# Performance work log

Hardware: AMD Instinct MI355X
Metric: run time of the kernel (lower is better)

## Reference

```python
import jax, jax.numpy as jnp
import numpy as np

N = 50000   # nodes
E = 800000  # edges


def gcn_conv(x, src, dst, W, b):
    # PyG GCNConv: h = x @ W; add self-loops; symmetric norm D^-1/2 A D^-1/2; + bias
    h = x @ W                                              # [N, dout]
    deg = jax.ops.segment_sum(jnp.ones((E,), h.dtype), dst, num_segments=N) + 1.0  # +1 self-loop
    inv_sqrt = jax.lax.rsqrt(deg)                          # [N]
    coef = inv_sqrt[src] * inv_sqrt[dst]                   # [E]
    agg = jax.ops.segment_sum(h[src] * coef[:, None], dst, num_segments=N)
    agg = agg + h * (inv_sqrt * inv_sqrt)[:, None]         # self-loop contribution
    return agg + b


def setup_inputs() -> dict:
    key = jax.random.key(0)
    ks = jax.random.split(key, 6)
    x = jax.random.normal(ks[0], (N, 128), jnp.float32)
    edge_index = jax.random.randint(ks[1], (2, E), 0, N, jnp.int32)
    W1 = jax.random.normal(ks[2], (128, 128), jnp.float32) * (1.0 / np.sqrt(128.0))
    b1 = jnp.zeros((128,), jnp.float32)
    W2 = jax.random.normal(ks[3], (128, 64), jnp.float32) * (1.0 / np.sqrt(128.0))
    b2 = jnp.zeros((64,), jnp.float32)
    return {"x": x, "edge_index": edge_index, "W1": W1, "b1": b1, "W2": W2, "b2": b2}


def reference(x, edge_index, W1, b1, W2, b2):
    src, dst = edge_index[0], edge_index[1]
    h = jax.nn.relu(gcn_conv(x, src, dst, W1, b1))
    # dropout is identity in eval mode (training=False)
    return gcn_conv(h, src, dst, W2, b2)
```

## Files before the change

kernel.cpp:

```cpp
#include <hip/hip_runtime.h>

typedef unsigned int uint32;
typedef unsigned short ushort16;

__device__ __forceinline__ ushort16 f2bf(float f) {
    union { float f; uint32 u; } v; v.f = f;
    uint32 r = v.u + 0x7fffu + ((v.u >> 16) & 1u);
    return (ushort16)(r >> 16);
}
__device__ __forceinline__ float bflo(uint32 u) {
    union { uint32 u; float f; } v; v.u = u << 16; return v.f;
}
__device__ __forceinline__ float bfhi(uint32 u) {
    union { uint32 u; float f; } v; v.u = u & 0xffff0000u; return v.f;
}

#define BSH 6
#define NBMAX 1024
#define CHUNK 4096


__global__ void k_zerob(int* __restrict__ b, int nb) {
    int i = blockIdx.x * 256 + threadIdx.x;
    if (i < nb) b[i] = 0;
}

__global__ __launch_bounds__(256) void k_bcount(const int* __restrict__ dst,
                                                int* __restrict__ bcnt, int e, int nb) {
    __shared__ int cnt[NBMAX];
    for (int i = threadIdx.x; i < nb; i += 256) cnt[i] = 0;
    __syncthreads();
    int base = blockIdx.x * CHUNK;
    int end = min(e, base + CHUNK);
    for (int i = base + threadIdx.x; i < end; i += 256)
        atomicAdd(&cnt[dst[i] >> BSH], 1);
    __syncthreads();
    for (int i = threadIdx.x; i < nb; i += 256) {
        int c = cnt[i];
        if (c) atomicAdd(&bcnt[i], c);
    }
}

__global__ void k_bscan(const int* __restrict__ bcnt, int* __restrict__ bstart,
                        int* __restrict__ bcur, int nb, int e) {
    __shared__ int s[256];
    __shared__ int carry;
    int tid = threadIdx.x;
    if (tid == 0) carry = 0;
    __syncthreads();
    for (int base = 0; base < nb; base += 256) {
        int v = (base + tid < nb) ? bcnt[base + tid] : 0;
        s[tid] = v;
        __syncthreads();
        for (int off = 1; off < 256; off <<= 1) {
            int t = (tid >= off) ? s[tid - off] : 0;
            __syncthreads();
            s[tid] += t;
            __syncthreads();
        }
        int ex = s[tid] - v + carry;
        if (base + tid < nb) { bstart[base + tid] = ex; bcur[base + tid] = ex; }
        __syncthreads();
        if (tid == 0) carry += s[255];
        __syncthreads();
    }
    if (tid == 0) bstart[nb] = e;
}

__global__ __launch_bounds__(256) void k_binA2(const int* __restrict__ src,
                                               const int* __restrict__ dst,
                                               int* __restrict__ bcur,
                                               int2* __restrict__ rec, int e, int nb) {
    __shared__ int cnt[NBMAX];
    __shared__ int bas[NBMAX];
    __shared__ int off[NBMAX];
    for (int i = threadIdx.x; i < nb; i += 256) { cnt[i] = 0; off[i] = 0; }
    __syncthreads();
    int base = blockIdx.x * CHUNK;
    int end = min(e, base + CHUNK);
    for (int i = base + threadIdx.x; i < end; i += 256)
        atomicAdd(&cnt[dst[i] >> BSH], 1);
    __syncthreads();
    for (int i = threadIdx.x; i < nb; i += 256) {
        int c = cnt[i];
        if (c) bas[i] = atomicAdd(&bcur[i], c);
    }
    __syncthreads();
    for (int i = base + threadIdx.x; i < end; i += 256) {
        int s = src[i];
        int d = dst[i];
        int b = d >> BSH;
        int p = bas[b] + atomicAdd(&off[b], 1);
        rec[p] = make_int2(s, d);
    }
}

__global__ __launch_bounds__(256) void k_degB(const int2* __restrict__ rec,
                                              const int* __restrict__ bstart,
                                              int* __restrict__ rowstart,
                                              float* __restrict__ inv, int n, int e) {
    __shared__ int cnt[64];
    int b = blockIdx.x;
    int st = bstart[b], en = bstart[b + 1];
    if (threadIdx.x < 64) cnt[threadIdx.x] = 0;
    __syncthreads();
    for (int i = st + threadIdx.x; i < en; i += 256)
        atomicAdd(&cnt[rec[i].y & 63], 1);
    __syncthreads();
    if (threadIdx.x < 64) {
        int c = cnt[threadIdx.x];
        int incl = c;
        #pragma unroll
        for (int o2 = 1; o2 < 64; o2 <<= 1) {
            int t = __shfl_up(incl, o2, 64);
            if ((int)threadIdx.x >= o2) incl += t;
        }
        int node = (b << BSH) + threadIdx.x;
        if (node < n) {
            rowstart[node] = st + incl - c;
            inv[node] = rsqrtf((float)c + 1.0f);
        }
    }
    if (b == 0 && threadIdx.x == 0) rowstart[n] = e;
}

__global__ __launch_bounds__(256) void k_fillB2(const int2* __restrict__ rec,
                                                const int* __restrict__ bstart,
                                                const int* __restrict__ rowstart,
                                                const float* __restrict__ inv,
                                                int2* __restrict__ es, int n) {
    __shared__ int cur[64];
    int b = blockIdx.x;
    int st = bstart[b], en = bstart[b + 1];
    if (threadIdx.x < 64) {
        int node = (b << BSH) + threadIdx.x;
        cur[threadIdx.x] = (node < n) ? (rowstart[node] - st) : 0;
    }
    __syncthreads();
    for (int i = st + threadIdx.x; i < en; i += 256) {
        int2 r = rec[i];
        int slot = atomicAdd(&cur[r.y & 63], 1);
        es[st + slot] = make_int2(r.x, __float_as_int(inv[r.x]));
    }
}


__global__ __launch_bounds__(256) void k_gemm1(const float* __restrict__ x,
                                               const float* __restrict__ W,
                                               ushort16* __restrict__ h, int n) {
    __shared__ float sW[128 * 128];
    __shared__ float sx[32 * 128];
    int tid = threadIdx.x;
    for (int i = tid * 4; i < 128 * 128; i += 1024)
        *(float4*)&sW[i] = *(const float4*)&W[i];
    int row0 = blockIdx.x * 32;
    for (int i = tid * 4; i < 32 * 128; i += 1024) {
        int r = row0 + (i >> 7);
        float4 v = (r < n) ? *(const float4*)&x[r * 128 + (i & 127)]
                           : make_float4(0.f, 0.f, 0.f, 0.f);
        *(float4*)&sx[i] = v;
    }
    __syncthreads();
    int c4 = (tid & 31) * 4;
    int rg = tid >> 5;
    float4 acc[4] = {};
    #pragma unroll 4
    for (int k = 0; k < 128; ++k) {
        float4 wv = *(const float4*)&sW[k * 128 + c4];
        #pragma unroll
        for (int i = 0; i < 4; ++i) {
            float xv = sx[(rg + 8 * i) * 128 + k];
            acc[i].x += xv * wv.x; acc[i].y += xv * wv.y;
            acc[i].z += xv * wv.z; acc[i].w += xv * wv.w;
        }
    }
    #pragma unroll
    for (int i = 0; i < 4; ++i) {
        int r = row0 + rg + 8 * i;
        if (r < n) {
            uint32 lo = (uint32)f2bf(acc[i].x) | ((uint32)f2bf(acc[i].y) << 16);
            uint32 hi = (uint32)f2bf(acc[i].z) | ((uint32)f2bf(acc[i].w) << 16);
            *(uint2*)&h[r * 128 + c4] = make_uint2(lo, hi);
        }
    }
}

__global__ __launch_bounds__(256) void k_gemm2(const float* __restrict__ a,
                                               const float* __restrict__ W,
                                               ushort16* __restrict__ h, int n) {
    __shared__ float sW[128 * 64];
    __shared__ float sx[64 * 128];
    int tid = threadIdx.x;
    for (int i = tid * 4; i < 128 * 64; i += 1024)
        *(float4*)&sW[i] = *(const float4*)&W[i];
    int row0 = blockIdx.x * 64;
    for (int i = tid * 4; i < 64 * 128; i += 1024) {
        int r = row0 + (i >> 7);
        float4 v = (r < n) ? *(const float4*)&a[r * 128 + (i & 127)]
                           : make_float4(0.f, 0.f, 0.f, 0.f);
        *(float4*)&sx[i] = v;
    }
    __syncthreads();
    int c4 = (tid & 15) * 4;
    int rg = tid >> 4;
    float4 acc[4] = {};
    #pragma unroll 4
    for (int k = 0; k < 128; ++k) {
        float4 wv = *(const float4*)&sW[k * 64 + c4];
        #pragma unroll
        for (int i = 0; i < 4; ++i) {
            float xv = sx[(rg + 16 * i) * 128 + k];
            acc[i].x += xv * wv.x; acc[i].y += xv * wv.y;
            acc[i].z += xv * wv.z; acc[i].w += xv * wv.w;
        }
    }
    #pragma unroll
    for (int i = 0; i < 4; ++i) {
        int r = row0 + rg + 16 * i;
        if (r < n) {
            uint32 lo = (uint32)f2bf(acc[i].x) | ((uint32)f2bf(acc[i].y) << 16);
            uint32 hi = (uint32)f2bf(acc[i].z) | ((uint32)f2bf(acc[i].w) << 16);
            *(uint2*)&h[r * 64 + c4] = make_uint2(lo, hi);
        }
    }
}

template <int COLS, bool RELU>
__global__ __launch_bounds__(256) void k_gather(const ushort16* __restrict__ h,
                                                const int* __restrict__ rowstart,
                                                const int2* __restrict__ es,
                                                const float* __restrict__ inv,
                                                const float* __restrict__ bias,
                                                float* __restrict__ out, int n) {
    int wave = threadIdx.x >> 6;
    int lane = threadIdx.x & 63;
    int node = blockIdx.x * 4 + wave;
    if (node >= n) return;
    int s0 = rowstart[node];
    int s1 = rowstart[node + 1];
    float iv = inv[node];

    if constexpr (COLS == 128) {
        int c = lane * 2;
        float accx = 0.f, accy = 0.f;
        int i = s0;
        for (; i + 8 <= s1; i += 8) {
            int   a[8];
            float w[8];
            uint32 u[8];
            #pragma unroll
            for (int j = 0; j < 8; ++j) {
                int2 r = es[i + j];
                a[j] = r.x;
                w[j] = __int_as_float(r.y);
            }
            #pragma unroll
            for (int j = 0; j < 8; ++j)
                u[j] = *(const uint32*)&h[(size_t)a[j] * 128 + c];
            #pragma unroll
            for (int j = 0; j < 8; ++j) {
                accx += w[j] * bflo(u[j]);
                accy += w[j] * bfhi(u[j]);
            }
        }
        for (; i < s1; ++i) {
            int2 r = es[i];
            uint32 u = *(const uint32*)&h[(size_t)r.x * 128 + c];
            float w = __int_as_float(r.y);
            accx += w * bflo(u);
            accy += w * bfhi(u);
        }
        uint32 us = *(const uint32*)&h[(size_t)node * 128 + c];
        float2 bb = *(const float2*)&bias[c];
        float ox = iv * accx + iv * iv * bflo(us) + bb.x;
        float oy = iv * accy + iv * iv * bfhi(us) + bb.y;
        if (RELU) { ox = fmaxf(ox, 0.f); oy = fmaxf(oy, 0.f); }
        *(float2*)&out[node * 128 + c] = make_float2(ox, oy);
    } else {
        int c = lane;
        float acc = 0.f;
        int i = s0;
        for (; i + 8 <= s1; i += 8) {
            int   a[8];
            float w[8];
            ushort16 u[8];
            #pragma unroll
            for (int j = 0; j < 8; ++j) {
                int2 r = es[i + j];
                a[j] = r.x;
                w[j] = __int_as_float(r.y);
            }
            #pragma unroll
            for (int j = 0; j < 8; ++j)
                u[j] = h[(size_t)a[j] * 64 + c];
            #pragma unroll
            for (int j = 0; j < 8; ++j)
                acc += w[j] * bflo((uint32)u[j]);
        }
        for (; i < s1; ++i) {
            int2 r = es[i];
            acc += __int_as_float(r.y) * bflo((uint32)h[(size_t)r.x * 64 + c]);
        }
        float self = bflo((uint32)h[(size_t)node * 64 + c]);
        float o = iv * acc + iv * iv * self + bias[c];
        if (RELU) o = fmaxf(o, 0.f);
        out[node * 64 + c] = o;
    }
}


extern "C" void kernel_launch(void* const* d_in, const int* in_sizes, int n_in,
                              void* d_out, int out_size, void* d_ws, size_t ws_size,
                              hipStream_t stream) {
    const float* x  = (const float*)d_in[0];
    const int*   ei = (const int*)d_in[1];
    const float* W1 = (const float*)d_in[2];
    const float* b1 = (const float*)d_in[3];
    const float* W2 = (const float*)d_in[4];
    const float* b2 = (const float*)d_in[5];
    float* out = (float*)d_out;

    const int N = in_sizes[0] / 128;
    const int E = in_sizes[1] / 2;
    const int NB = (N + 63) >> BSH;
    const int* src = ei;
    const int* dstp = ei + E;

    char* p = (char*)d_ws;
    auto take = [&](size_t bytes) {
        char* r = p;
        p += (bytes + 255) & ~(size_t)255;
        return r;
    };
    float*    inv      = (float*)take((size_t)N * 4);
    int*      rowstart = (int*)take((size_t)(N + 1) * 4);
    int*      bcnt     = (int*)take((size_t)NB * 4);
    int*      bstart   = (int*)take((size_t)(NB + 1) * 4);
    int*      bcur     = (int*)take((size_t)NB * 4);
    int2*     rec      = (int2*)take((size_t)E * 8);
    int2*     es       = (int2*)take((size_t)E * 8);
    ushort16* h1       = (ushort16*)take((size_t)N * 128 * 2);
    float*    act1     = (float*)take((size_t)N * 128 * 4);
    ushort16* h2       = (ushort16*)h1;

    const int nbC = (E + CHUNK - 1) / CHUNK;

    k_zerob <<<(NB + 255) / 256, 256, 0, stream>>>(bcnt, NB);
    k_bcount<<<nbC, 256, 0, stream>>>(dstp, bcnt, E, NB);
    k_bscan <<<1, 256, 0, stream>>>(bcnt, bstart, bcur, NB, E);
    k_binA2 <<<nbC, 256, 0, stream>>>(src, dstp, bcur, rec, E, NB);
    k_degB  <<<NB, 256, 0, stream>>>(rec, bstart, rowstart, inv, N, E);
    k_fillB2<<<NB, 256, 0, stream>>>(rec, bstart, rowstart, inv, es, N);

    k_gemm1<<<(N + 31) / 32, 256, 0, stream>>>(x, W1, h1, N);
    k_gather<128, true><<<(N + 3) / 4, 256, 0, stream>>>(h1, rowstart, es, inv, b1, act1, N);
    k_gemm2<<<(N + 63) / 64, 256, 0, stream>>>(act1, W2, h2, N);
    k_gather<64, false><<<(N + 3) / 4, 256, 0, stream>>>(h2, rowstart, es, inv, b2, out, N);
}
```

Baseline: 259.5 us.

## Replace scalar FP32 GEMMs with split-bf16 MFMA GEMMs

```diff
diff --git a/kernel.cpp b/kernel.cpp
--- a/kernel.cpp
+++ b/kernel.cpp
@@ -1,17 +1,19 @@
 #include <hip/hip_runtime.h>
 
 typedef unsigned int uint32;
-typedef unsigned short ushort16;
-
-__device__ __forceinline__ ushort16 f2bf(float f) {
+typedef unsigned short ush;
+typedef __attribute__((ext_vector_type(8))) short short8;
+typedef __attribute__((ext_vector_type(4))) float f32x4;
+
+__device__ __forceinline__ ush f2bf(float f) {
     union { float f; uint32 u; } v; v.f = f;
     uint32 r = v.u + 0x7fffu + ((v.u >> 16) & 1u);
-    return (ushort16)(r >> 16);
-}
-__device__ __forceinline__ float bflo(uint32 u) {
+    return (ush)(r >> 16);
+}
+__device__ __forceinline__ float bfl(uint32 u) {
     union { uint32 u; float f; } v; v.u = u << 16; return v.f;
 }
-__device__ __forceinline__ float bfhi(uint32 u) {
+__device__ __forceinline__ float bfh(uint32 u) {
     union { uint32 u; float f; } v; v.u = u & 0xffff0000u; return v.f;
 }
 
@@ -144,89 +146,120 @@
     }
 }
 
-
-__global__ __launch_bounds__(256) void k_gemm1(const float* __restrict__ x,
-                                               const float* __restrict__ W,
-                                               ushort16* __restrict__ h, int n) {
-    __shared__ float sW[128 * 128];
-    __shared__ float sx[32 * 128];
+__global__ void k_wcvt(const float* __restrict__ W, ush* __restrict__ wh,
+                       ush* __restrict__ wl, int csh, int total) {
+    int i = blockIdx.x * 256 + threadIdx.x;
+    if (i >= total) return;
+    int k = i >> csh;
+    int col = i & ((1 << csh) - 1);
+    float w = W[i];
+    ush hi = f2bf(w);
+    ush lo = f2bf(w - bfl((uint32)hi));
+    int byte = ((col * 128 + k) * 2) ^ ((col & 7) << 4);
+    *(ush*)((char*)wh + byte) = hi;
+    *(ush*)((char*)wl + byte) = lo;
+}
+
+template <int COUT>
+__global__ __launch_bounds__(256) void k_gemm_mfma(const float* __restrict__ x,
+                                                   const ush* __restrict__ gwh,
+                                                   const ush* __restrict__ gwl,
+                                                   ush* __restrict__ h, int n) {
+    constexpr int CT = COUT / 32;
+    __shared__ short xh[128 * 128];
+    __shared__ short xl[128 * 128];
+    __shared__ short wh[COUT * 128];
+    __shared__ short wl[COUT * 128];
     int tid = threadIdx.x;
-    for (int i = tid * 4; i < 128 * 128; i += 1024)
-        *(float4*)&sW[i] = *(const float4*)&W[i];
-    int row0 = blockIdx.x * 32;
-    for (int i = tid * 4; i < 32 * 128; i += 1024) {
-        int r = row0 + (i >> 7);
-        float4 v = (r < n) ? *(const float4*)&x[r * 128 + (i & 127)]
-                           : make_float4(0.f, 0.f, 0.f, 0.f);
-        *(float4*)&sx[i] = v;
-    }
-    __syncthreads();
-    int c4 = (tid & 31) * 4;
-    int rg = tid >> 5;
-    float4 acc[4] = {};
-    #pragma unroll 4
-    for (int k = 0; k < 128; ++k) {
-        float4 wv = *(const float4*)&sW[k * 128 + c4];
-        #pragma unroll
-        for (int i = 0; i < 4; ++i) {
-            float xv = sx[(rg + 8 * i) * 128 + k];
-            acc[i].x += xv * wv.x; acc[i].y += xv * wv.y;
-            acc[i].z += xv * wv.z; acc[i].w += xv * wv.w;
-        }
+    int row0 = blockIdx.x * 128;
+
+    for (int i = tid; i < COUT * 16; i += 256) {
+        ((short8*)wh)[i] = ((const short8*)gwh)[i];
+        ((short8*)wl)[i] = ((const short8*)gwl)[i];
     }
     #pragma unroll
-    for (int i = 0; i < 4; ++i) {
-        int r = row0 + rg + 8 * i;
-        if (r < n) {
-            uint32 lo = (uint32)f2bf(acc[i].x) | ((uint32)f2bf(acc[i].y) << 16);
-            uint32 hi = (uint32)f2bf(acc[i].z) | ((uint32)f2bf(acc[i].w) << 16);
-            *(uint2*)&h[r * 128 + c4] = make_uint2(lo, hi);
-        }
-    }
-}
-
-__global__ __launch_bounds__(256) void k_gemm2(const float* __restrict__ a,
-                                               const float* __restrict__ W,
-                                               ushort16* __restrict__ h, int n) {
-    __shared__ float sW[128 * 64];
-    __shared__ float sx[64 * 128];
-    int tid = threadIdx.x;
-    for (int i = tid * 4; i < 128 * 64; i += 1024)
-        *(float4*)&sW[i] = *(const float4*)&W[i];
-    int row0 = blockIdx.x * 64;
-    for (int i = tid * 4; i < 64 * 128; i += 1024) {
-        int r = row0 + (i >> 7);
-        float4 v = (r < n) ? *(const float4*)&a[r * 128 + (i & 127)]
-                           : make_float4(0.f, 0.f, 0.f, 0.f);
-        *(float4*)&sx[i] = v;
-    }
-    __syncthreads();
-    int c4 = (tid & 15) * 4;
-    int rg = tid >> 4;
-    float4 acc[4] = {};
-    #pragma unroll 4
-    for (int k = 0; k < 128; ++k) {
-        float4 wv = *(const float4*)&sW[k * 64 + c4];
-        #pragma unroll
-        for (int i = 0; i < 4; ++i) {
-            float xv = sx[(rg + 16 * i) * 128 + k];
-            acc[i].x += xv * wv.x; acc[i].y += xv * wv.y;
-            acc[i].z += xv * wv.z; acc[i].w += xv * wv.w;
-        }
-    }
+    for (int i = 0; i < 8; ++i) {
+        int rl = (tid >> 4) + i * 16;
+        int k0 = (tid & 15) * 8;
+        int row = row0 + rl;
+        float f[8];
+        if (row < n) {
+            float4 p0 = *(const float4*)&x[(size_t)row * 128 + k0];
+            float4 p1 = *(const float4*)&x[(size_t)row * 128 + k0 + 4];
+            f[0] = p0.x; f[1] = p0.y; f[2] = p0.z; f[3] = p0.w;
+            f[4] = p1.x; f[5] = p1.y; f[6] = p1.z; f[7] = p1.w;
+        } else {
+            #pragma unroll
+            for (int j = 0; j < 8; ++j) f[j] = 0.f;
+        }
+        short8 hi, lo;
+        #pragma unroll
+        for (int j = 0; j < 8; ++j) {
+            ush hb = f2bf(f[j]);
+            hi[j] = (short)hb;
+            lo[j] = (short)f2bf(f[j] - bfl((uint32)hb));
+        }
+        int byte = (rl * 256 + k0 * 2) ^ ((rl & 7) << 4);
+        *(short8*)((char*)xh + byte) = hi;
+        *(short8*)((char*)xl + byte) = lo;
+    }
+    __syncthreads();
+
+    int wid = tid >> 6, lane = tid & 63;
+    int wr = wid >> 1, wc = wid & 1;
+    int arow = wr * 64;
+    int bcol = wc * (COUT / 2);
+    int l15 = lane & 15, kg = lane >> 4;
+
+    f32x4 acc[4][CT];
     #pragma unroll
-    for (int i = 0; i < 4; ++i) {
-        int r = row0 + rg + 16 * i;
-        if (r < n) {
-            uint32 lo = (uint32)f2bf(acc[i].x) | ((uint32)f2bf(acc[i].y) << 16);
-            uint32 hi = (uint32)f2bf(acc[i].z) | ((uint32)f2bf(acc[i].w) << 16);
-            *(uint2*)&h[r * 64 + c4] = make_uint2(lo, hi);
+    for (int rt = 0; rt < 4; ++rt)
+        #pragma unroll
+        for (int ct = 0; ct < CT; ++ct)
+            acc[rt][ct] = (f32x4){0.f, 0.f, 0.f, 0.f};
+
+    #pragma unroll
+    for (int ks = 0; ks < 4; ++ks) {
+        short8 ah[4], al[4];
+        #pragma unroll
+        for (int rt = 0; rt < 4; ++rt) {
+            int r = arow + rt * 16 + l15;
+            int byte = (r * 256 + ks * 64 + kg * 16) ^ ((r & 7) << 4);
+            ah[rt] = *(const short8*)((const char*)xh + byte);
+            al[rt] = *(const short8*)((const char*)xl + byte);
+        }
+        #pragma unroll
+        for (int ct = 0; ct < CT; ++ct) {
+            int c = bcol + ct * 16 + l15;
+            int byte = (c * 256 + ks * 64 + kg * 16) ^ ((c & 7) << 4);
+            short8 bh = *(const short8*)((const char*)wh + byte);
+            short8 bl = *(const short8*)((const char*)wl + byte);
+            #pragma unroll
+            for (int rt = 0; rt < 4; ++rt) {
+                acc[rt][ct] = __builtin_amdgcn_mfma_f32_16x16x32_bf16(ah[rt], bh, acc[rt][ct], 0, 0, 0);
+                acc[rt][ct] = __builtin_amdgcn_mfma_f32_16x16x32_bf16(al[rt], bh, acc[rt][ct], 0, 0, 0);
+                acc[rt][ct] = __builtin_amdgcn_mfma_f32_16x16x32_bf16(ah[rt], bl, acc[rt][ct], 0, 0, 0);
+            }
+        }
+    }
+
+    int rq = kg * 4;
+    #pragma unroll
+    for (int rt = 0; rt < 4; ++rt) {
+        #pragma unroll
+        for (int ct = 0; ct < CT; ++ct) {
+            int col = bcol + ct * 16 + l15;
+            #pragma unroll
+            for (int q = 0; q < 4; ++q) {
+                int row = row0 + arow + rt * 16 + rq + q;
+                if (row < n) h[(size_t)row * COUT + col] = f2bf(acc[rt][ct][q]);
+            }
         }
     }
 }
 
 template <int COLS, bool RELU>
-__global__ __launch_bounds__(256) void k_gather(const ushort16* __restrict__ h,
+__global__ __launch_bounds__(256) void k_gather(const ush* __restrict__ h,
                                                 const int* __restrict__ rowstart,
                                                 const int2* __restrict__ es,
                                                 const float* __restrict__ inv,
@@ -245,8 +278,8 @@
         float accx = 0.f, accy = 0.f;
         int i = s0;
         for (; i + 8 <= s1; i += 8) {
-            int   a[8];
-            float w[8];
+            int    a[8];
+            float  w[8];
             uint32 u[8];
             #pragma unroll
             for (int j = 0; j < 8; ++j) {
@@ -259,21 +292,21 @@
                 u[j] = *(const uint32*)&h[(size_t)a[j] * 128 + c];
             #pragma unroll
             for (int j = 0; j < 8; ++j) {
-                accx += w[j] * bflo(u[j]);
-                accy += w[j] * bfhi(u[j]);
+                accx += w[j] * bfl(u[j]);
+                accy += w[j] * bfh(u[j]);
             }
         }
         for (; i < s1; ++i) {
             int2 r = es[i];
             uint32 u = *(const uint32*)&h[(size_t)r.x * 128 + c];
             float w = __int_as_float(r.y);
-            accx += w * bflo(u);
-            accy += w * bfhi(u);
+            accx += w * bfl(u);
+            accy += w * bfh(u);
         }
         uint32 us = *(const uint32*)&h[(size_t)node * 128 + c];
         float2 bb = *(const float2*)&bias[c];
-        float ox = iv * accx + iv * iv * bflo(us) + bb.x;
-        float oy = iv * accy + iv * iv * bfhi(us) + bb.y;
+        float ox = iv * accx + iv * iv * bfl(us) + bb.x;
+        float oy = iv * accy + iv * iv * bfh(us) + bb.y;
         if (RELU) { ox = fmaxf(ox, 0.f); oy = fmaxf(oy, 0.f); }
         *(float2*)&out[node * 128 + c] = make_float2(ox, oy);
     } else {
@@ -283,7 +316,7 @@
         for (; i + 8 <= s1; i += 8) {
             int   a[8];
             float w[8];
-            ushort16 u[8];
+            ush   u[8];
             #pragma unroll
             for (int j = 0; j < 8; ++j) {
                 int2 r = es[i + j];
@@ -295,13 +328,13 @@
                 u[j] = h[(size_t)a[j] * 64 + c];
             #pragma unroll
             for (int j = 0; j < 8; ++j)
-                acc += w[j] * bflo((uint32)u[j]);
+                acc += w[j] * bfl((uint32)u[j]);
         }
         for (; i < s1; ++i) {
             int2 r = es[i];
-            acc += __int_as_float(r.y) * bflo((uint32)h[(size_t)r.x * 64 + c]);
-        }
-        float self = bflo((uint32)h[(size_t)node * 64 + c]);
+            acc += __int_as_float(r.y) * bfl((uint32)h[(size_t)r.x * 64 + c]);
+        }
+        float self = bfl((uint32)h[(size_t)node * 64 + c]);
         float o = iv * acc + iv * iv * self + bias[c];
         if (RELU) o = fmaxf(o, 0.f);
         out[node * 64 + c] = o;
@@ -332,16 +365,20 @@
         p += (bytes + 255) & ~(size_t)255;
         return r;
     };
-    float*    inv      = (float*)take((size_t)N * 4);
-    int*      rowstart = (int*)take((size_t)(N + 1) * 4);
-    int*      bcnt     = (int*)take((size_t)NB * 4);
-    int*      bstart   = (int*)take((size_t)(NB + 1) * 4);
-    int*      bcur     = (int*)take((size_t)NB * 4);
-    int2*     rec      = (int2*)take((size_t)E * 8);
-    int2*     es       = (int2*)take((size_t)E * 8);
-    ushort16* h1       = (ushort16*)take((size_t)N * 128 * 2);
-    float*    act1     = (float*)take((size_t)N * 128 * 4);
-    ushort16* h2       = (ushort16*)h1;
+    float* inv      = (float*)take((size_t)N * 4);
+    int*   rowstart = (int*)take((size_t)(N + 1) * 4);
+    int*   bcnt     = (int*)take((size_t)NB * 4);
+    int*   bstart   = (int*)take((size_t)(NB + 1) * 4);
+    int*   bcur     = (int*)take((size_t)NB * 4);
+    int2*  rec      = (int2*)take((size_t)E * 8);
+    int2*  es       = (int2*)take((size_t)E * 8);
+    ush*   w1h      = (ush*)take(16384 * 2);
+    ush*   w1l      = (ush*)take(16384 * 2);
+    ush*   w2h      = (ush*)take(8192 * 2);
+    ush*   w2l      = (ush*)take(8192 * 2);
+    ush*   h1       = (ush*)take((size_t)N * 128 * 2);
+    float* act1     = (float*)take((size_t)N * 128 * 4);
+    ush*   h2       = h1;
 
     const int nbC = (E + CHUNK - 1) / CHUNK;
 
@@ -352,8 +389,12 @@
     k_degB  <<<NB, 256, 0, stream>>>(rec, bstart, rowstart, inv, N, E);
     k_fillB2<<<NB, 256, 0, stream>>>(rec, bstart, rowstart, inv, es, N);
 
-    k_gemm1<<<(N + 31) / 32, 256, 0, stream>>>(x, W1, h1, N);
+    k_wcvt<<<64, 256, 0, stream>>>(W1, w1h, w1l, 7, 16384);
+    k_wcvt<<<32, 256, 0, stream>>>(W2, w2h, w2l, 6, 8192);
+
+    const int gb = (N + 127) / 128;
+    k_gemm_mfma<128><<<gb, 256, 0, stream>>>(x, w1h, w1l, h1, N);
     k_gather<128, true><<<(N + 3) / 4, 256, 0, stream>>>(h1, rowstart, es, inv, b1, act1, N);
-    k_gemm2<<<(N + 63) / 64, 256, 0, stream>>>(act1, W2, h2, N);
+    k_gemm_mfma<64><<<gb, 256, 0, stream>>>(act1, w2h, w2l, h2, N);
     k_gather<64, false><<<(N + 3) / 4, 256, 0, stream>>>(h2, rowstart, es, inv, b2, out, N);
 }
```

Measured after the change: 240.1 us. 7.5% less time.
